# Optimization experiments

Hardware: AMD Instinct MI355X
Metric: run time of the kernel (lower is better)

The kernel has to match this reference:

```python
import jax, jax.numpy as jnp
import numpy as np

B, S, D_IN, D_EMB = 16, 8192, 256, 256
LEVELS = 8  # pywt default max level for db1 with signal length 256: log2(256)
INV_SQRT2 = np.float32(1.0 / np.sqrt(2.0))


def haar_wavedec_concat(x, levels):
    """Multi-level Haar (db1) DWT along last axis; returns coeffs concatenated
    in pywt order [cA_L, cD_L, ..., cD_1]. Assumes last dim = 2**levels,
    so 'symmetric' padding is a no-op (filter length 2, even lengths).
    pywt db1 convention: cA[k]=(x[2k]+x[2k+1])/sqrt2, cD[k]=(x[2k]-x[2k+1])/sqrt2.
    """
    details = []
    a = x
    for _ in range(levels):
        even = a[..., ::2]
        odd = a[..., 1::2]
        details.append((even - odd) * INV_SQRT2)
        a = (even + odd) * INV_SQRT2
    return jnp.concatenate([a] + details[::-1], axis=-1)


def setup_inputs() -> dict:
    key = jax.random.key(0)
    k_x, k_w, k_b = jax.random.split(key, 3)
    x = jax.random.normal(k_x, (B, S, D_IN), dtype=jnp.float32)
    # nn.Linear(input_dim, embed_dim): W is (embed_dim, input_dim)
    bound = np.float32(1.0 / np.sqrt(D_IN))
    W = jax.random.uniform(k_w, (D_EMB, D_IN), dtype=jnp.float32, minval=-bound, maxval=bound)
    b = jax.random.uniform(k_b, (D_EMB,), dtype=jnp.float32, minval=-bound, maxval=bound)
    return {"x": x, "W": W, "b": b}


def reference(x, W, b):
    coeffs = haar_wavedec_concat(x, LEVELS)  # (B, S, D_IN)
    # concatenated coeff length == D_IN exactly, so no pad/trim (matches original no-op branch)
    return jnp.einsum('bsd,ed->bse', coeffs, W) + b
```

## Files before the change

kernel.cpp:

```cpp
#include <hip/hip_runtime.h>
#include <hip/hip_bf16.h>

typedef short short8 __attribute__((ext_vector_type(8)));
typedef float f32x4 __attribute__((ext_vector_type(4)));

#define INV_SQRT2F 0.70710678118654752440f

__device__ __forceinline__ unsigned short f2bf(float f) {
  union { float f; unsigned u; } v; v.f = f;
  unsigned u = v.u;
  unsigned r = (u + 0x7FFFu + ((u >> 16) & 1u)) >> 16;
  return (unsigned short)r;
}

__global__ void haar_pack(const float* __restrict__ W, unsigned short* __restrict__ Wp) {
  __shared__ float cbuf[4][256];
  __shared__ float buf0[4][256];
  __shared__ float buf1[4][256];
  const int tid = threadIdx.x;
  const int w = tid >> 6, l = tid & 63;
  const int e = blockIdx.x * 4 + w;
  const float* row = W + e * 256;
  for (int k = l; k < 256; k += 64) cbuf[w][k] = row[k];
  __syncthreads();
  if (l == 0) buf0[w][0] = cbuf[w][0];
  __syncthreads();
  float* A = buf0[w];
  float* Bv = buf1[w];
  int len = 1;
  for (int s = 0; s < 8; ++s) {
    for (int k = l; k < len; k += 64) {
      float av = A[k], dv = cbuf[w][len + k];
      Bv[2 * k]     = (av + dv) * INV_SQRT2F;
      Bv[2 * k + 1] = (av - dv) * INV_SQRT2F;
    }
    __syncthreads();
    float* t = A; A = Bv; Bv = t;
    len <<= 1;
  }
  const int nblk = e >> 4, lr = e & 15;
  for (int k = l; k < 256; k += 64) {
    int kk = k >> 5, win = k & 31, lhi = win >> 3, j = win & 7;
    int lane = lhi * 16 + lr;
    Wp[(((nblk * 8 + kk) * 64 + lane) << 3) + j] = f2bf(A[k]);
  }
}

#define NTILES 16
#define BM 32

__global__ __launch_bounds__(512, 2) void wemb_gemm(
    const float* __restrict__ x, const unsigned short* __restrict__ Wp,
    const float* __restrict__ bias, float* __restrict__ out) {
  __shared__ char bl[131072];
  __shared__ char al[16384];
  const int tid = threadIdx.x;

  {
    const ulonglong2* s = (const ulonglong2*)Wp;
    ulonglong2* d = (ulonglong2*)bl;
#pragma unroll
    for (int i = 0; i < 16; ++i) d[i * 512 + tid] = s[i * 512 + tid];
  }

  const int w = tid >> 6, lane = tid & 63;
  const int wm = w >> 2, wn = w & 3;
  const int lr = lane & 15, lhi = lane >> 4;

  float bv[4];
#pragma unroll
  for (int n = 0; n < 4; ++n) bv[n] = bias[wn * 64 + n * 16 + lr];

  const long tile0 = (long)blockIdx.x * NTILES;

  {
    const float4* src = (const float4*)(x + tile0 * (BM * 256));
#pragma unroll
    for (int i = 0; i < 4; ++i) {
      int f = i * 512 + tid;
      float4 v = src[f];
      int row = f >> 6, colb = (f & 63) * 8;
      ushort4 p; p.x = f2bf(v.x); p.y = f2bf(v.y); p.z = f2bf(v.z); p.w = f2bf(v.w);
      *(ushort4*)(al + row * 512 + (colb ^ ((row & 7) << 4))) = p;
    }
  }
  __syncthreads();

#pragma unroll 1
  for (int it = 0; it < NTILES; ++it) {
    const long tt = tile0 + it;

    float4 pf[4];
    if (it < NTILES - 1) {
      const float4* src = (const float4*)(x + (tt + 1) * (BM * 256));
#pragma unroll
      for (int i = 0; i < 4; ++i) pf[i] = src[i * 512 + tid];
    }

    f32x4 acc[4];
#pragma unroll
    for (int n = 0; n < 4; ++n) acc[n] = (f32x4){0.f, 0.f, 0.f, 0.f};
#pragma unroll
    for (int kk = 0; kk < 8; ++kk) {
      const int arow = wm * 16 + lr;
      const int colb = (kk * 32 + lhi * 8) * 2;
      short8 a = *(const short8*)(al + arow * 512 + (colb ^ ((arow & 7) << 4)));
#pragma unroll
      for (int n = 0; n < 4; ++n) {
        short8 b = *(const short8*)(bl + ((((wn * 4 + n) * 8 + kk) * 64 + lane) << 4));
        acc[n] = __builtin_amdgcn_mfma_f32_16x16x32_bf16(a, b, acc[n], 0, 0, 0);
      }
    }

    {
      float* orow = out + (tt * BM + wm * 16 + lhi * 4) * 256;
#pragma unroll
      for (int n = 0; n < 4; ++n) {
        const int e = wn * 64 + n * 16 + lr;
#pragma unroll
        for (int r = 0; r < 4; ++r) orow[r * 256 + e] = acc[n][r] + bv[n];
      }
    }

    __syncthreads();
    if (it < NTILES - 1) {
#pragma unroll
      for (int i = 0; i < 4; ++i) {
        int f = i * 512 + tid;
        int row = f >> 6, colb = (f & 63) * 8;
        ushort4 p; p.x = f2bf(pf[i].x); p.y = f2bf(pf[i].y); p.z = f2bf(pf[i].z); p.w = f2bf(pf[i].w);
        *(ushort4*)(al + row * 512 + (colb ^ ((row & 7) << 4))) = p;
      }
    }
    __syncthreads();
  }
}

extern "C" void kernel_launch(void* const* d_in, const int* in_sizes, int n_in,
                              void* d_out, int out_size, void* d_ws, size_t ws_size,
                              hipStream_t stream) {
  const float* x = (const float*)d_in[0];
  const float* W = (const float*)d_in[1];
  const float* b = (const float*)d_in[2];
  float* out = (float*)d_out;
  unsigned short* Wp = (unsigned short*)d_ws;

  haar_pack<<<64, 256, 0, stream>>>(W, Wp);

  const int grid = (out_size / 256) / (BM * NTILES);
  wemb_gemm<<<grid, 512, 0, stream>>>(x, Wp, b, out);
}
```

Baseline: 58.12 us.

## Keep W fragments in registers, double-buffer A tile, use nontemporal output stores

The packed Haar-transformed weight is no longer copied into 128KB of shared memory. Each wave now loads its 32 short8 B fragments directly into registers once. The A tile in LDS is double-buffered, which removes one __syncthreads per iteration, and output stores become nontemporal. This cuts LDS use enough to allow more blocks per CU and removes the per-MFMA LDS reads of B, at the cost of about 128 extra VGPRs per thread, which may cause spills or limit occupancy under launch_bounds(512,2).

```diff
diff --git a/kernel.cpp b/kernel.cpp
--- a/kernel.cpp
+++ b/kernel.cpp
@@ -52,20 +52,18 @@
 __global__ __launch_bounds__(512, 2) void wemb_gemm(
     const float* __restrict__ x, const unsigned short* __restrict__ Wp,
     const float* __restrict__ bias, float* __restrict__ out) {
-  __shared__ char bl[131072];
-  __shared__ char al[16384];
+  __shared__ char al[2][16384];
   const int tid = threadIdx.x;
-
-  {
-    const ulonglong2* s = (const ulonglong2*)Wp;
-    ulonglong2* d = (ulonglong2*)bl;
-#pragma unroll
-    for (int i = 0; i < 16; ++i) d[i * 512 + tid] = s[i * 512 + tid];
-  }
-
   const int w = tid >> 6, lane = tid & 63;
   const int wm = w >> 2, wn = w & 3;
   const int lr = lane & 15, lhi = lane >> 4;
+
+  short8 Bf[8][4];
+#pragma unroll
+  for (int kk = 0; kk < 8; ++kk)
+#pragma unroll
+    for (int n = 0; n < 4; ++n)
+      Bf[kk][n] = *(const short8*)(Wp + ((((wn * 4 + n) * 8 + kk) * 64 + lane) << 3));
 
   float bv[4];
 #pragma unroll
@@ -81,7 +79,7 @@
       float4 v = src[f];
       int row = f >> 6, colb = (f & 63) * 8;
       ushort4 p; p.x = f2bf(v.x); p.y = f2bf(v.y); p.z = f2bf(v.z); p.w = f2bf(v.w);
-      *(ushort4*)(al + row * 512 + (colb ^ ((row & 7) << 4))) = p;
+      *(ushort4*)(al[0] + row * 512 + (colb ^ ((row & 7) << 4))) = p;
     }
   }
   __syncthreads();
@@ -89,6 +87,8 @@
 #pragma unroll 1
   for (int it = 0; it < NTILES; ++it) {
     const long tt = tile0 + it;
+    char* cur = al[it & 1];
+    char* nxt = al[(it & 1) ^ 1];
 
     float4 pf[4];
     if (it < NTILES - 1) {
@@ -104,12 +104,10 @@
     for (int kk = 0; kk < 8; ++kk) {
       const int arow = wm * 16 + lr;
       const int colb = (kk * 32 + lhi * 8) * 2;
-      short8 a = *(const short8*)(al + arow * 512 + (colb ^ ((arow & 7) << 4)));
+      short8 a = *(const short8*)(cur + arow * 512 + (colb ^ ((arow & 7) << 4)));
 #pragma unroll
-      for (int n = 0; n < 4; ++n) {
-        short8 b = *(const short8*)(bl + ((((wn * 4 + n) * 8 + kk) * 64 + lane) << 4));
-        acc[n] = __builtin_amdgcn_mfma_f32_16x16x32_bf16(a, b, acc[n], 0, 0, 0);
-      }
+      for (int n = 0; n < 4; ++n)
+        acc[n] = __builtin_amdgcn_mfma_f32_16x16x32_bf16(a, Bf[kk][n], acc[n], 0, 0, 0);
     }
 
     {
@@ -118,18 +116,18 @@
       for (int n = 0; n < 4; ++n) {
         const int e = wn * 64 + n * 16 + lr;
 #pragma unroll
-        for (int r = 0; r < 4; ++r) orow[r * 256 + e] = acc[n][r] + bv[n];
+        for (int r = 0; r < 4; ++r)
+          __builtin_nontemporal_store(acc[n][r] + bv[n], orow + r * 256 + e);
       }
     }
 
-    __syncthreads();
     if (it < NTILES - 1) {
 #pragma unroll
       for (int i = 0; i < 4; ++i) {
         int f = i * 512 + tid;
         int row = f >> 6, colb = (f & 63) * 8;
         ushort4 p; p.x = f2bf(pf[i].x); p.y = f2bf(pf[i].y); p.z = f2bf(pf[i].z); p.w = f2bf(pf[i].w);
-        *(ushort4*)(al + row * 512 + (colb ^ ((row & 7) << 4))) = p;
+        *(ushort4*)(nxt + row * 512 + (colb ^ ((row & 7) << 4))) = p;
       }
     }
     __syncthreads();
```

After: 64.91 us. 1.12x slower.
